# Kernel tuning notes

Measured on AMD Instinct MI355X. Metric: run time of the kernel, lower is better.

The kernel has to match this reference:

```python
import jax, jax.numpy as jnp
import numpy as np

B, C, N, T = 8, 256, 1024, 60
TW = 12  # time window size
BN_EPS = 1e-5


def _B_matrix():
    # Block-diagonal window mask: three 12x12 blocks, then one 24x24 block.
    A = np.zeros((T, T), dtype=np.float32)
    for k in range(3):
        A[k * TW:(k + 1) * TW, k * TW:(k + 1) * TW] = 1.0
    A[3 * TW:3 * TW + 2 * TW, 3 * TW:3 * TW + 2 * TW] = 1.0
    return jnp.asarray(-1e13 * (1.0 - A), dtype=jnp.float32)


def setup_inputs() -> dict:
    key = jax.random.key(0)
    ks = jax.random.split(key, 5)
    return {
        "seq": jax.random.normal(ks[0], (B, C, N, T), dtype=jnp.float32),
        "w1": jax.random.normal(ks[1], (C,), dtype=jnp.float32) * 0.05,   # conv1 weight (c_in -> 1)
        "w2": jax.random.normal(ks[2], (N,), dtype=jnp.float32) * 0.02,   # conv2 weight (num_nodes -> 1)
        "w": jax.random.normal(ks[3], (N, C), dtype=jnp.float32) * 0.03,  # xavier-ish scale
        "b": jnp.zeros((T, T), dtype=jnp.float32),
        "v": jax.random.normal(ks[4], (T, T), dtype=jnp.float32) * 0.1,
        "gamma": jnp.ones((T,), dtype=jnp.float32),
        "beta": jnp.zeros((T,), dtype=jnp.float32),
    }


def reference(seq, w1, w2, w, b, v, gamma, beta):
    # seq: [B, C, N, T]
    # conv1 over channel dim on seq.permute(0,1,3,2): f1[b,t,n] = sum_c w1[c]*seq[b,c,n,t]
    f1 = jnp.einsum('c,bcnt->btn', w1, seq)            # [B, T, N]
    # conv2 over node dim on seq.permute(0,2,1,3): f2[b,c,t] = sum_n w2[n]*seq[b,c,n,t]
    f2 = jnp.einsum('n,bcnt->bct', w2, seq)            # [B, C, T]
    logits = jax.nn.sigmoid(jnp.einsum('btn,nc,bcs->bts', f1, w, f2) + b)  # [B, T, T]
    logits = jnp.einsum('ij,bjt->bit', v, logits)      # v @ logits
    # BatchNorm1d (training mode, biased var) over channels = dim 2 after permute
    x = jnp.transpose(logits, (0, 2, 1))               # [B, T(chan), T]
    mean = x.mean(axis=(0, 2), keepdims=True)
    var = x.var(axis=(0, 2), keepdims=True)
    x = (x - mean) * jax.lax.rsqrt(var + BN_EPS) * gamma[None, :, None] + beta[None, :, None]
    logits = jnp.transpose(x, (0, 2, 1))               # [B, T, T]
    return jax.nn.softmax(logits + _B_matrix(), axis=-1)
```

## Files before the change

### kernel.cpp

```cpp
#include <hip/hip_runtime.h>
#include <cstdint>
#include <cstddef>


#define CSTRIDE 61440

typedef float vfloat4 __attribute__((ext_vector_type(4)));

__device__ __forceinline__ float quad_reduce(float x) {
    int y1 = __builtin_amdgcn_update_dpp(0, __float_as_int(x), 0xB1, 0xF, 0xF, true);
    float s1 = x + __int_as_float(y1);
    int y2 = __builtin_amdgcn_update_dpp(0, __float_as_int(s1), 0x4E, 0xF, 0xF, true);
    return s1 + __int_as_float(y2);
}

__global__ __launch_bounds__(256) void kA(const float* __restrict__ seq,
                                          const float* __restrict__ w1,
                                          const float* __restrict__ w2,
                                          float* __restrict__ f1p,
                                          float* __restrict__ f2p) {
    const int blk  = blockIdx.x;
    const int b    = blk >> 7;
    const int cg   = (blk >> 4) & 7;
    const int nc   = blk & 15;
    const int tid  = threadIdx.x;
    const int wv   = tid >> 6;
    const int lane = tid & 63;
    const int q    = lane & 3;
    const int r    = lane >> 2;
    const bool act = (r < 15);
    const int base_n = (nc << 6) + (wv << 4);
    const int c0   = cg << 5;

    __shared__ float lf2[7680];

    float w2v[4];
    #pragma unroll
    for (int j = 0; j < 4; ++j) w2v[j] = w2[base_n + 4 * j + q];

    const size_t planeOff = (size_t)(b * 256 + c0) * CSTRIDE + (size_t)((base_n + q) * 60 + 4 * r);
    const float* p0 = seq + planeOff;
    const float* p1 = p0 + (size_t)CSTRIDE;
    const float* p2 = p0 + 2 * (size_t)CSTRIDE;
    const float* p3 = p0 + 3 * (size_t)CSTRIDE;

    vfloat4 P0[4], P1[4], P2[4], P3[4];
    #pragma unroll
    for (int j = 0; j < 4; ++j) {
        P0[j] = (vfloat4)(0.f);
        P1[j] = P0[j]; P2[j] = P0[j]; P3[j] = P0[j];
    }
    if (act) {
        #pragma unroll
        for (int j = 0; j < 4; ++j) P0[j] = __builtin_nontemporal_load((const vfloat4*)(p0 + j * 240));
        #pragma unroll
        for (int j = 0; j < 4; ++j) P1[j] = __builtin_nontemporal_load((const vfloat4*)(p1 + j * 240));
        #pragma unroll
        for (int j = 0; j < 4; ++j) P2[j] = __builtin_nontemporal_load((const vfloat4*)(p2 + j * 240));
        #pragma unroll
        for (int j = 0; j < 4; ++j) P3[j] = __builtin_nontemporal_load((const vfloat4*)(p3 + j * 240));
    }
    p0 += 4 * (size_t)CSTRIDE;
    p1 += 4 * (size_t)CSTRIDE;
    p2 += 4 * (size_t)CSTRIDE;
    p3 += 4 * (size_t)CSTRIDE;

    vfloat4 acc[4];
    #pragma unroll
    for (int j = 0; j < 4; ++j) acc[j] = (vfloat4)(0.f);

#define KA_STEP(P, S, PP)                                                               \
    {                                                                                   \
        const int cc = (ii << 2) + (S);                                                 \
        const float wc = w1[c0 + cc];                                                   \
        _Pragma("unroll")                                                               \
        for (int j = 0; j < 4; ++j) acc[j] += wc * P[j];                                \
        vfloat4 f2v = w2v[0]*P[0] + w2v[1]*P[1] + w2v[2]*P[2] + w2v[3]*P[3];            \
        if (pref) {                                                                     \
            _Pragma("unroll")                                                           \
            for (int j = 0; j < 4; ++j)                                                 \
                P[j] = __builtin_nontemporal_load((const vfloat4*)((PP) + j * 240));    \
        }                                                                               \
        f2v.x = quad_reduce(f2v.x);                                                     \
        f2v.y = quad_reduce(f2v.y);                                                     \
        f2v.z = quad_reduce(f2v.z);                                                     \
        f2v.w = quad_reduce(f2v.w);                                                     \
        if (act && q == 0) {                                                            \
            *(vfloat4*)(&lf2[(cc * 4 + wv) * 60 + 4 * r]) = f2v;                        \
        }                                                                               \
    }

    for (int ii = 0; ii < 8; ++ii) {
        const bool pref = act && (ii < 7);
        KA_STEP(P0, 0, p0)
        KA_STEP(P1, 1, p1)
        KA_STEP(P2, 2, p2)
        KA_STEP(P3, 3, p3)
        p0 += 4 * (size_t)CSTRIDE;
        p1 += 4 * (size_t)CSTRIDE;
        p2 += 4 * (size_t)CSTRIDE;
        p3 += 4 * (size_t)CSTRIDE;
    }
#undef KA_STEP

    if (act) {
        float* dst = f1p + ((size_t)((cg * 8 + b) * 60 + 4 * r)) * 1024 + base_n + q;
        #pragma unroll
        for (int j = 0; j < 4; ++j) {
            dst[0 * 1024 + 4 * j] = acc[j].x;
            dst[1 * 1024 + 4 * j] = acc[j].y;
            dst[2 * 1024 + 4 * j] = acc[j].z;
            dst[3 * 1024 + 4 * j] = acc[j].w;
        }
    }

    __syncthreads();
    #pragma unroll
    for (int k = 0; k < 2; ++k) {
        const int id4 = tid + k * 256;
        if (id4 < 480) {
            const int cc = id4 / 15;
            const int p  = id4 - cc * 15;
            vfloat4 s = (vfloat4)(0.f);
            #pragma unroll
            for (int w = 0; w < 4; ++w)
                s += *(const vfloat4*)(&lf2[(cc * 4 + w) * 60 + 4 * p]);
            *(vfloat4*)(f2p + ((size_t)(b * 256 + c0 + cc) * 16 + nc) * 60 + 4 * p) = s;
        }
    }
}

__global__ __launch_bounds__(256) void K1(const float* __restrict__ f2p,
                                          const float* __restrict__ f1p,
                                          const float* __restrict__ w,
                                          float* __restrict__ f2,
                                          float* __restrict__ g1p) {
    const int blk = blockIdx.x;
    const int tid = threadIdx.x;
    if (blk < 512) {
        const int row = blk * 4 + (tid >> 6);
        const int t   = tid & 63;
        if (t >= 60) return;
        const float* src = f2p + (size_t)row * 960 + t;
        float s = 0.f;
        #pragma unroll
        for (int k = 0; k < 16; ++k) s += src[k * 60];
        f2[(size_t)row * 60 + t] = s;
    } else {
        const int blk2 = blk - 512;
        const int b    = blk2 / 60;
        const int rem  = blk2 % 60;
        const int tg   = rem >> 2;
        const int ks   = rem & 3;
        const int c    = tid;

        __shared__ float fl[1024];

        {
            const int row  = tid >> 6;
            const int col4 = tid & 63;
            const int t    = tg * 4 + row;
            vfloat4 s = (vfloat4)(0.f);
            #pragma unroll
            for (int g = 0; g < 8; ++g)
                s += *(const vfloat4*)(f1p + ((size_t)((g * 8 + b) * 60 + t)) * 1024
                                             + (ks << 8) + 4 * col4);
            *(vfloat4*)(&fl[(row << 8) + 4 * col4]) = s;
        }
        __syncthreads();

        float a0 = 0.f, a1 = 0.f, a2 = 0.f, a3 = 0.f;
        const float* wp = w + (size_t)(ks << 8) * 256 + c;
        #pragma unroll 4
        for (int n = 0; n < 256; ++n) {
            const float wv = wp[n * 256];
            a0 += fl[n] * wv;
            a1 += fl[256 + n] * wv;
            a2 += fl[512 + n] * wv;
            a3 += fl[768 + n] * wv;
        }
        float* dst = g1p + ((size_t)((ks * 8 + b) * 60 + tg * 4)) * 256 + c;
        dst[0]   = a0;
        dst[256] = a1;
        dst[512] = a2;
        dst[768] = a3;
    }
}

__global__ __launch_bounds__(256) void kD(const float* __restrict__ g1p,
                                          const float* __restrict__ f2,
                                          const float* __restrict__ bmat,
                                          float* __restrict__ logits) {
    const int bt = blockIdx.x;
    const int b  = bt / 60;
    const int t  = bt % 60;
    const int tid = threadIdx.x;
    const int cq = tid >> 6;
    const int s  = tid & 63;

    __shared__ float f2s[15364];
    __shared__ float g1r[256];
    __shared__ float red[256];

    const float* fsrc = f2 + (size_t)b * 15360;
    #pragma unroll
    for (int k = 0; k < 15; ++k) {
        const int idx = tid + k * 256;
        *(float4*)(&f2s[4 * idx]) = *(const float4*)(fsrc + 4 * idx);
    }
    if (tid < 64) {
        vfloat4 sg = (vfloat4)(0.f);
        #pragma unroll
        for (int ks = 0; ks < 4; ++ks)
            sg += *(const vfloat4*)(g1p + ((size_t)((ks * 8 + b) * 60 + t)) * 256 + 4 * tid);
        *(vfloat4*)(&g1r[4 * tid]) = sg;
    }
    __syncthreads();

    float acc = 0.f;
    #pragma unroll 8
    for (int cc = 0; cc < 64; ++cc) {
        const int c = cq * 64 + cc;
        acc += g1r[c] * f2s[c * 60 + s];
    }
    red[tid] = acc;
    __syncthreads();
    if (tid < 60) {
        const float x = red[tid] + red[64 + tid] + red[128 + tid] + red[192 + tid]
                      + bmat[t * 60 + tid];
        logits[(size_t)bt * 60 + tid] = 1.f / (1.f + __expf(-x));
    }
}

__global__ __launch_bounds__(256) void kE(const float* __restrict__ v,
                                          const float* __restrict__ logits,
                                          float* __restrict__ l2) {
    const int bi = blockIdx.x;
    const int b  = bi / 60;
    const int i  = bi % 60;
    const int tid = threadIdx.x;

    __shared__ float L[3600];
    const float* src = logits + (size_t)b * 3600;
    #pragma unroll
    for (int k = 0; k < 3; ++k) {
        const int idx = tid + k * 256;
        *(float4*)(&L[4 * idx]) = *(const float4*)(src + 4 * idx);
    }
    if (tid < 132) {
        const int idx = tid + 768;
        *(float4*)(&L[4 * idx]) = *(const float4*)(src + 4 * idx);
    }
    __syncthreads();

    if (tid < 60) {
        float acc = 0.f;
        #pragma unroll 4
        for (int j = 0; j < 60; ++j) acc += v[i * 60 + j] * L[j * 60 + tid];
        l2[(size_t)bi * 60 + tid] = acc;
    }
}

__global__ __launch_bounds__(256) void kG(const float* __restrict__ l2,
                                          const float* __restrict__ gamma,
                                          const float* __restrict__ beta,
                                          float* __restrict__ out) {
    const int bi = blockIdx.x;
    const int i  = bi % 60;
    const int tid = threadIdx.x;

    __shared__ float ps[240];
    __shared__ float pss[240];
    __shared__ float sm[60];
    __shared__ float sr[60];

    if (tid < 240) {
        const int t = tid % 60;
        const int m = tid / 60;
        float s = 0.f, ss = 0.f;
        const float* src = l2 + (size_t)(m * 120) * 60 + t;
        #pragma unroll 8
        for (int k = 0; k < 120; ++k) {
            const float x = src[k * 60];
            s  += x;
            ss += x * x;
        }
        ps[tid]  = s;
        pss[tid] = ss;
    }
    __syncthreads();
    if (tid < 60) {
        const float s   = ps[tid] + ps[60 + tid] + ps[120 + tid] + ps[180 + tid];
        const float ss  = pss[tid] + pss[60 + tid] + pss[120 + tid] + pss[180 + tid];
        const float m   = s * (1.f / 480.f);
        const float var = ss * (1.f / 480.f) - m * m;
        sm[tid] = m;
        sr[tid] = rsqrtf(var + 1e-5f);
    }
    __syncthreads();

    if (tid < 64) {
        const int t = tid;
        float x = -3.0e38f;
        if (t < 60) {
            const float val = l2[(size_t)bi * 60 + t];
            const float y   = (val - sm[t]) * sr[t] * gamma[t] + beta[t];
            const int  br   = (i < 36) ? (i / 12) : 3;
            const int  lo   = (br < 3) ? br * 12 : 36;
            const int  hi   = (br < 3) ? lo + 12 : 60;
            const bool valid = (t >= lo) && (t < hi);
            x = valid ? y : (y - 1e13f);
        }
        float mx = x;
        #pragma unroll
        for (int o = 32; o > 0; o >>= 1) mx = fmaxf(mx, __shfl_xor(mx, o));
        float e = 0.f;
        if (t < 60) e = __expf(x - mx);
        float smn = e;
        #pragma unroll
        for (int o = 32; o > 0; o >>= 1) smn += __shfl_xor(smn, o);
        if (t < 60) out[(size_t)bi * 60 + t] = e / smn;
    }
}

extern "C" void kernel_launch(void* const* d_in, const int* in_sizes, int n_in,
                              void* d_out, int out_size, void* d_ws, size_t ws_size,
                              hipStream_t stream) {
    const float* seq   = (const float*)d_in[0];
    const float* w1    = (const float*)d_in[1];
    const float* w2    = (const float*)d_in[2];
    const float* w     = (const float*)d_in[3];
    const float* bmat  = (const float*)d_in[4];
    const float* v     = (const float*)d_in[5];
    const float* gamma = (const float*)d_in[6];
    const float* beta  = (const float*)d_in[7];
    float* out = (float*)d_out;
    float* ws  = (float*)d_ws;

    float* f1p    = ws;
    float* f2p    = ws + 3932160;
    float* f2     = ws + 5898240;
    float* g1p    = ws + 6021120;
    float* logits = ws + 6512640;
    float* l2     = ws + 6541440;

    kA<<<1024, 256, 0, stream>>>(seq, w1, w2, f1p, f2p);
    K1<<<992, 256, 0, stream>>>(f2p, f1p, w, f2, g1p);
    kD<<<480, 256, 0, stream>>>(g1p, f2, bmat, logits);
    kE<<<480, 256, 0, stream>>>(v, logits, l2);
    kG<<<480, 256, 0, stream>>>(l2, gamma, beta, out);
}
```

Measured before the change: 131.8 us.

## Fuse four tail kernels into one cooperative kernel with grid syncs

Replaces the K1, kD, kE and kG launches with a single cooperative kernel that uses grid.sync() between stages, removing three kernel launch gaps. The kD stage no longer stages the per-batch f2 slab in shared memory and instead reads it directly from global memory. Shared memory is unioned into one 3600-float buffer. This relies on all 992 blocks being co-resident (launch bounds of 4 blocks per CU are declared). Grid-wide barriers add their own overhead, and the direct global reads of f2 may cost more than the old shared-memory staging.

```diff
diff --git a/kernel.cpp b/kernel.cpp
--- a/kernel.cpp
+++ b/kernel.cpp
@@ -1,6 +1,9 @@
 #include <hip/hip_runtime.h>
+#include <hip/hip_cooperative_groups.h>
 #include <cstdint>
 #include <cstddef>
+
+namespace cg = cooperative_groups;
 
 
 #define CSTRIDE 61440
@@ -21,7 +24,7 @@
                                           float* __restrict__ f2p) {
     const int blk  = blockIdx.x;
     const int b    = blk >> 7;
-    const int cg   = (blk >> 4) & 7;
+    const int cg_  = (blk >> 4) & 7;
     const int nc   = blk & 15;
     const int tid  = threadIdx.x;
     const int wv   = tid >> 6;
@@ -30,7 +33,7 @@
     const int r    = lane >> 2;
     const bool act = (r < 15);
     const int base_n = (nc << 6) + (wv << 4);
-    const int c0   = cg << 5;
+    const int c0   = cg_ << 5;
 
     __shared__ float lf2[7680];
 
@@ -104,7 +107,7 @@
 #undef KA_STEP
 
     if (act) {
-        float* dst = f1p + ((size_t)((cg * 8 + b) * 60 + 4 * r)) * 1024 + base_n + q;
+        float* dst = f1p + ((size_t)((cg_ * 8 + b) * 60 + 4 * r)) * 1024 + base_n + q;
         #pragma unroll
         for (int j = 0; j < 4; ++j) {
             dst[0 * 1024 + 4 * j] = acc[j].x;
@@ -123,29 +126,40 @@
             const int p  = id4 - cc * 15;
             vfloat4 s = (vfloat4)(0.f);
             #pragma unroll
-            for (int w = 0; w < 4; ++w)
-                s += *(const vfloat4*)(&lf2[(cc * 4 + w) * 60 + 4 * p]);
+            for (int w_ = 0; w_ < 4; ++w_)
+                s += *(const vfloat4*)(&lf2[(cc * 4 + w_) * 60 + 4 * p]);
             *(vfloat4*)(f2p + ((size_t)(b * 256 + c0 + cc) * 16 + nc) * 60 + 4 * p) = s;
         }
     }
 }
 
-__global__ __launch_bounds__(256) void K1(const float* __restrict__ f2p,
-                                          const float* __restrict__ f1p,
-                                          const float* __restrict__ w,
-                                          float* __restrict__ f2,
-                                          float* __restrict__ g1p) {
+__global__ __launch_bounds__(256, 4) void KT(const float* __restrict__ f2p,
+                                             const float* __restrict__ f1p,
+                                             const float* __restrict__ w,
+                                             const float* __restrict__ bmat,
+                                             const float* __restrict__ v,
+                                             const float* __restrict__ gamma,
+                                             const float* __restrict__ beta,
+                                             float* __restrict__ f2,
+                                             float* __restrict__ g1p,
+                                             float* __restrict__ logits,
+                                             float* __restrict__ l2,
+                                             float* __restrict__ out) {
+    cg::grid_group grid = cg::this_grid();
+    __shared__ float S[3600];
     const int blk = blockIdx.x;
     const int tid = threadIdx.x;
+
     if (blk < 512) {
         const int row = blk * 4 + (tid >> 6);
         const int t   = tid & 63;
-        if (t >= 60) return;
-        const float* src = f2p + (size_t)row * 960 + t;
-        float s = 0.f;
-        #pragma unroll
-        for (int k = 0; k < 16; ++k) s += src[k * 60];
-        f2[(size_t)row * 60 + t] = s;
+        if (t < 60) {
+            const float* src = f2p + (size_t)row * 960 + t;
+            float s = 0.f;
+            #pragma unroll
+            for (int k = 0; k < 16; ++k) s += src[k * 60];
+            f2[(size_t)row * 60 + t] = s;
+        }
     } else {
         const int blk2 = blk - 512;
         const int b    = blk2 / 60;
@@ -154,8 +168,6 @@
         const int ks   = rem & 3;
         const int c    = tid;
 
-        __shared__ float fl[1024];
-
         {
             const int row  = tid >> 6;
             const int col4 = tid & 63;
@@ -165,7 +177,7 @@
             for (int g = 0; g < 8; ++g)
                 s += *(const vfloat4*)(f1p + ((size_t)((g * 8 + b) * 60 + t)) * 1024
                                              + (ks << 8) + 4 * col4);
-            *(vfloat4*)(&fl[(row << 8) + 4 * col4]) = s;
+            *(vfloat4*)(&S[(row << 8) + 4 * col4]) = s;
         }
         __syncthreads();
 
@@ -174,10 +186,10 @@
         #pragma unroll 4
         for (int n = 0; n < 256; ++n) {
             const float wv = wp[n * 256];
-            a0 += fl[n] * wv;
-            a1 += fl[256 + n] * wv;
-            a2 += fl[512 + n] * wv;
-            a3 += fl[768 + n] * wv;
+            a0 += S[n] * wv;
+            a1 += S[256 + n] * wv;
+            a2 += S[512 + n] * wv;
+            a3 += S[768 + n] * wv;
         }
         float* dst = g1p + ((size_t)((ks * 8 + b) * 60 + tg * 4)) * 256 + c;
         dst[0]   = a0;
@@ -185,141 +197,113 @@
         dst[512] = a2;
         dst[768] = a3;
     }
-}
-
-__global__ __launch_bounds__(256) void kD(const float* __restrict__ g1p,
-                                          const float* __restrict__ f2,
-                                          const float* __restrict__ bmat,
-                                          float* __restrict__ logits) {
-    const int bt = blockIdx.x;
-    const int b  = bt / 60;
-    const int t  = bt % 60;
-    const int tid = threadIdx.x;
-    const int cq = tid >> 6;
-    const int s  = tid & 63;
-
-    __shared__ float f2s[15364];
-    __shared__ float g1r[256];
-    __shared__ float red[256];
-
-    const float* fsrc = f2 + (size_t)b * 15360;
-    #pragma unroll
-    for (int k = 0; k < 15; ++k) {
-        const int idx = tid + k * 256;
-        *(float4*)(&f2s[4 * idx]) = *(const float4*)(fsrc + 4 * idx);
-    }
-    if (tid < 64) {
-        vfloat4 sg = (vfloat4)(0.f);
-        #pragma unroll
-        for (int ks = 0; ks < 4; ++ks)
-            sg += *(const vfloat4*)(g1p + ((size_t)((ks * 8 + b) * 60 + t)) * 256 + 4 * tid);
-        *(vfloat4*)(&g1r[4 * tid]) = sg;
-    }
-    __syncthreads();
-
-    float acc = 0.f;
-    #pragma unroll 8
-    for (int cc = 0; cc < 64; ++cc) {
-        const int c = cq * 64 + cc;
-        acc += g1r[c] * f2s[c * 60 + s];
-    }
-    red[tid] = acc;
-    __syncthreads();
-    if (tid < 60) {
-        const float x = red[tid] + red[64 + tid] + red[128 + tid] + red[192 + tid]
-                      + bmat[t * 60 + tid];
-        logits[(size_t)bt * 60 + tid] = 1.f / (1.f + __expf(-x));
-    }
-}
-
-__global__ __launch_bounds__(256) void kE(const float* __restrict__ v,
-                                          const float* __restrict__ logits,
-                                          float* __restrict__ l2) {
-    const int bi = blockIdx.x;
-    const int b  = bi / 60;
-    const int i  = bi % 60;
-    const int tid = threadIdx.x;
-
-    __shared__ float L[3600];
-    const float* src = logits + (size_t)b * 3600;
-    #pragma unroll
-    for (int k = 0; k < 3; ++k) {
-        const int idx = tid + k * 256;
-        *(float4*)(&L[4 * idx]) = *(const float4*)(src + 4 * idx);
-    }
-    if (tid < 132) {
-        const int idx = tid + 768;
-        *(float4*)(&L[4 * idx]) = *(const float4*)(src + 4 * idx);
-    }
-    __syncthreads();
-
-    if (tid < 60) {
+    grid.sync();
+
+    if (blk < 480) {
+        const int b  = blk / 60;
+        const int t  = blk % 60;
+        const int cq = tid >> 6;
+        const int s  = tid & 63;
+
+        if (tid < 64) {
+            vfloat4 sg = (vfloat4)(0.f);
+            #pragma unroll
+            for (int ks = 0; ks < 4; ++ks)
+                sg += *(const vfloat4*)(g1p + ((size_t)((ks * 8 + b) * 60 + t)) * 256 + 4 * tid);
+            *(vfloat4*)(&S[4 * tid]) = sg;
+        }
+        __syncthreads();
+
         float acc = 0.f;
-        #pragma unroll 4
-        for (int j = 0; j < 60; ++j) acc += v[i * 60 + j] * L[j * 60 + tid];
-        l2[(size_t)bi * 60 + tid] = acc;
-    }
-}
-
-__global__ __launch_bounds__(256) void kG(const float* __restrict__ l2,
-                                          const float* __restrict__ gamma,
-                                          const float* __restrict__ beta,
-                                          float* __restrict__ out) {
-    const int bi = blockIdx.x;
-    const int i  = bi % 60;
-    const int tid = threadIdx.x;
-
-    __shared__ float ps[240];
-    __shared__ float pss[240];
-    __shared__ float sm[60];
-    __shared__ float sr[60];
-
-    if (tid < 240) {
-        const int t = tid % 60;
-        const int m = tid / 60;
-        float s = 0.f, ss = 0.f;
-        const float* src = l2 + (size_t)(m * 120) * 60 + t;
+        const float* fb = f2 + (size_t)b * 15360;
         #pragma unroll 8
-        for (int k = 0; k < 120; ++k) {
-            const float x = src[k * 60];
-            s  += x;
-            ss += x * x;
-        }
-        ps[tid]  = s;
-        pss[tid] = ss;
-    }
-    __syncthreads();
-    if (tid < 60) {
-        const float s   = ps[tid] + ps[60 + tid] + ps[120 + tid] + ps[180 + tid];
-        const float ss  = pss[tid] + pss[60 + tid] + pss[120 + tid] + pss[180 + tid];
-        const float m   = s * (1.f / 480.f);
-        const float var = ss * (1.f / 480.f) - m * m;
-        sm[tid] = m;
-        sr[tid] = rsqrtf(var + 1e-5f);
-    }
-    __syncthreads();
-
-    if (tid < 64) {
-        const int t = tid;
-        float x = -3.0e38f;
-        if (t < 60) {
-            const float val = l2[(size_t)bi * 60 + t];
-            const float y   = (val - sm[t]) * sr[t] * gamma[t] + beta[t];
-            const int  br   = (i < 36) ? (i / 12) : 3;
-            const int  lo   = (br < 3) ? br * 12 : 36;
-            const int  hi   = (br < 3) ? lo + 12 : 60;
-            const bool valid = (t >= lo) && (t < hi);
-            x = valid ? y : (y - 1e13f);
-        }
-        float mx = x;
-        #pragma unroll
-        for (int o = 32; o > 0; o >>= 1) mx = fmaxf(mx, __shfl_xor(mx, o));
-        float e = 0.f;
-        if (t < 60) e = __expf(x - mx);
-        float smn = e;
-        #pragma unroll
-        for (int o = 32; o > 0; o >>= 1) smn += __shfl_xor(smn, o);
-        if (t < 60) out[(size_t)bi * 60 + t] = e / smn;
+        for (int cc = 0; cc < 64; ++cc) {
+            const int c = cq * 64 + cc;
+            acc += S[c] * fb[c * 60 + s];
+        }
+        S[512 + tid] = acc;
+        __syncthreads();
+        if (tid < 60) {
+            const float x = S[512 + tid] + S[576 + tid] + S[640 + tid] + S[704 + tid]
+                          + bmat[t * 60 + tid];
+            logits[(size_t)blk * 60 + tid] = 1.f / (1.f + __expf(-x));
+        }
+    }
+    grid.sync();
+
+    if (blk < 480) {
+        const int b = blk / 60;
+        const int i = blk % 60;
+        const float* src = logits + (size_t)b * 3600;
+        #pragma unroll
+        for (int k = 0; k < 3; ++k) {
+            const int idx = tid + k * 256;
+            *(vfloat4*)(&S[4 * idx]) = *(const vfloat4*)(src + 4 * idx);
+        }
+        if (tid < 132) {
+            const int idx = tid + 768;
+            *(vfloat4*)(&S[4 * idx]) = *(const vfloat4*)(src + 4 * idx);
+        }
+        __syncthreads();
+
+        if (tid < 60) {
+            float acc = 0.f;
+            #pragma unroll 4
+            for (int j = 0; j < 60; ++j) acc += v[i * 60 + j] * S[j * 60 + tid];
+            l2[(size_t)blk * 60 + tid] = acc;
+        }
+    }
+    grid.sync();
+
+    if (blk < 480) {
+        const int i = blk % 60;
+        if (tid < 240) {
+            const int t = tid % 60;
+            const int m = tid / 60;
+            float s = 0.f, ss = 0.f;
+            const float* src = l2 + (size_t)(m * 120) * 60 + t;
+            #pragma unroll 8
+            for (int k = 0; k < 120; ++k) {
+                const float x = src[k * 60];
+                s  += x;
+                ss += x * x;
+            }
+            S[tid]       = s;
+            S[240 + tid] = ss;
+        }
+        __syncthreads();
+        if (tid < 60) {
+            const float s   = S[tid] + S[60 + tid] + S[120 + tid] + S[180 + tid];
+            const float ss  = S[240 + tid] + S[300 + tid] + S[360 + tid] + S[420 + tid];
+            const float m   = s * (1.f / 480.f);
+            const float var = ss * (1.f / 480.f) - m * m;
+            S[480 + tid] = m;
+            S[540 + tid] = rsqrtf(var + 1e-5f);
+        }
+        __syncthreads();
+
+        if (tid < 64) {
+            const int t = tid;
+            float x = -3.0e38f;
+            if (t < 60) {
+                const float val = l2[(size_t)blk * 60 + t];
+                const float y   = (val - S[480 + t]) * S[540 + t] * gamma[t] + beta[t];
+                const int  br   = (i < 36) ? (i / 12) : 3;
+                const int  lo   = (br < 3) ? br * 12 : 36;
+                const int  hi   = (br < 3) ? lo + 12 : 60;
+                const bool valid = (t >= lo) && (t < hi);
+                x = valid ? y : (y - 1e13f);
+            }
+            float mx = x;
+            #pragma unroll
+            for (int o = 32; o > 0; o >>= 1) mx = fmaxf(mx, __shfl_xor(mx, o));
+            float e = 0.f;
+            if (t < 60) e = __expf(x - mx);
+            float smn = e;
+            #pragma unroll
+            for (int o = 32; o > 0; o >>= 1) smn += __shfl_xor(smn, o);
+            if (t < 60) out[(size_t)blk * 60 + t] = e / smn;
+        }
     }
 }
 
@@ -345,8 +329,9 @@
     float* l2     = ws + 6541440;
 
     kA<<<1024, 256, 0, stream>>>(seq, w1, w2, f1p, f2p);
-    K1<<<992, 256, 0, stream>>>(f2p, f1p, w, f2, g1p);
-    kD<<<480, 256, 0, stream>>>(g1p, f2, bmat, logits);
-    kE<<<480, 256, 0, stream>>>(v, logits, l2);
-    kG<<<480, 256, 0, stream>>>(l2, gamma, beta, out);
+
+    void* args[] = { (void*)&f2p, (void*)&f1p, (void*)&w, (void*)&bmat, (void*)&v,
+                     (void*)&gamma, (void*)&beta, (void*)&f2, (void*)&g1p,
+                     (void*)&logits, (void*)&l2, (void*)&out };
+    hipLaunchCooperativeKernel((const void*)KT, dim3(992), dim3(256), args, 0, stream);
 }
```

Measured after the change: 470.1 us. +256.8%, slower.

## Fuse sigmoid-logits and v-matmul kernels into one per-batch column-chunk kernel

Applied to the files above, without the earlier changes.

Merges kD and kE into a single kernel, kDE, launched with 32 blocks. Each block handles one batch and a 15-column slice of t. The block stages f2 transposed in shared memory, computes the sigmoid logits for all 60 rows in four chunks of 16, then applies v @ S for its columns. This removes one launch and the intermediate logits round trip to global memory. In exchange, the grid drops from 480 blocks to 32, so far fewer CUs are used, and each block serially re-reads g1p from global memory.

```diff
diff --git a/kernel.cpp b/kernel.cpp
--- a/kernel.cpp
+++ b/kernel.cpp
@@ -21,7 +21,7 @@
                                           float* __restrict__ f2p) {
     const int blk  = blockIdx.x;
     const int b    = blk >> 7;
-    const int cg   = (blk >> 4) & 7;
+    const int cg_  = (blk >> 4) & 7;
     const int nc   = blk & 15;
     const int tid  = threadIdx.x;
     const int wv   = tid >> 6;
@@ -30,7 +30,7 @@
     const int r    = lane >> 2;
     const bool act = (r < 15);
     const int base_n = (nc << 6) + (wv << 4);
-    const int c0   = cg << 5;
+    const int c0   = cg_ << 5;
 
     __shared__ float lf2[7680];
 
@@ -104,7 +104,7 @@
 #undef KA_STEP
 
     if (act) {
-        float* dst = f1p + ((size_t)((cg * 8 + b) * 60 + 4 * r)) * 1024 + base_n + q;
+        float* dst = f1p + ((size_t)((cg_ * 8 + b) * 60 + 4 * r)) * 1024 + base_n + q;
         #pragma unroll
         for (int j = 0; j < 4; ++j) {
             dst[0 * 1024 + 4 * j] = acc[j].x;
@@ -123,8 +123,8 @@
             const int p  = id4 - cc * 15;
             vfloat4 s = (vfloat4)(0.f);
             #pragma unroll
-            for (int w = 0; w < 4; ++w)
-                s += *(const vfloat4*)(&lf2[(cc * 4 + w) * 60 + 4 * p]);
+            for (int w_ = 0; w_ < 4; ++w_)
+                s += *(const vfloat4*)(&lf2[(cc * 4 + w_) * 60 + 4 * p]);
             *(vfloat4*)(f2p + ((size_t)(b * 256 + c0 + cc) * 16 + nc) * 60 + 4 * p) = s;
         }
     }
@@ -187,77 +187,75 @@
     }
 }
 
-__global__ __launch_bounds__(256) void kD(const float* __restrict__ g1p,
-                                          const float* __restrict__ f2,
-                                          const float* __restrict__ bmat,
-                                          float* __restrict__ logits) {
-    const int bt = blockIdx.x;
-    const int b  = bt / 60;
-    const int t  = bt % 60;
-    const int tid = threadIdx.x;
-    const int cq = tid >> 6;
-    const int s  = tid & 63;
-
-    __shared__ float f2s[15364];
-    __shared__ float g1r[256];
-    __shared__ float red[256];
-
-    const float* fsrc = f2 + (size_t)b * 15360;
+__global__ __launch_bounds__(256) void kDE(const float* __restrict__ g1p,
+                                           const float* __restrict__ f2,
+                                           const float* __restrict__ bmat,
+                                           const float* __restrict__ v,
+                                           float* __restrict__ l2) {
+    const int blk   = blockIdx.x;
+    const int b     = blk >> 2;
+    const int tc    = blk & 3;
+    const int tbase = tc * 15;
+    const int tid   = threadIdx.x;
+
+    __shared__ float F[15][260];
+    __shared__ float Gr[16][264];
+    __shared__ float S[60][16];
+
     #pragma unroll
     for (int k = 0; k < 15; ++k) {
         const int idx = tid + k * 256;
-        *(float4*)(&f2s[4 * idx]) = *(const float4*)(fsrc + 4 * idx);
-    }
-    if (tid < 64) {
-        vfloat4 sg = (vfloat4)(0.f);
-        #pragma unroll
-        for (int ks = 0; ks < 4; ++ks)
-            sg += *(const vfloat4*)(g1p + ((size_t)((ks * 8 + b) * 60 + t)) * 256 + 4 * tid);
-        *(vfloat4*)(&g1r[4 * tid]) = sg;
+        const int c   = idx / 15;
+        const int tp  = idx % 15;
+        F[tp][c] = f2[(size_t)b * 15360 + c * 60 + tbase + tp];
     }
     __syncthreads();
 
-    float acc = 0.f;
-    #pragma unroll 8
-    for (int cc = 0; cc < 64; ++cc) {
-        const int c = cq * 64 + cc;
-        acc += g1r[c] * f2s[c * 60 + s];
-    }
-    red[tid] = acc;
-    __syncthreads();
-    if (tid < 60) {
-        const float x = red[tid] + red[64 + tid] + red[128 + tid] + red[192 + tid]
-                      + bmat[t * 60 + tid];
-        logits[(size_t)bt * 60 + tid] = 1.f / (1.f + __expf(-x));
-    }
-}
-
-__global__ __launch_bounds__(256) void kE(const float* __restrict__ v,
-                                          const float* __restrict__ logits,
-                                          float* __restrict__ l2) {
-    const int bi = blockIdx.x;
-    const int b  = bi / 60;
-    const int i  = bi % 60;
-    const int tid = threadIdx.x;
-
-    __shared__ float L[3600];
-    const float* src = logits + (size_t)b * 3600;
-    #pragma unroll
-    for (int k = 0; k < 3; ++k) {
-        const int idx = tid + k * 256;
-        *(float4*)(&L[4 * idx]) = *(const float4*)(src + 4 * idx);
-    }
-    if (tid < 132) {
-        const int idx = tid + 768;
-        *(float4*)(&L[4 * idx]) = *(const float4*)(src + 4 * idx);
-    }
-    __syncthreads();
-
-    if (tid < 60) {
-        float acc = 0.f;
-        #pragma unroll 4
-        for (int j = 0; j < 60; ++j) acc += v[i * 60 + j] * L[j * 60 + tid];
-        l2[(size_t)bi * 60 + tid] = acc;
+    const int jl = tid / 15;
+    const int tp = tid % 15;
+
+    for (int jb = 0; jb < 4; ++jb) {
+        #pragma unroll
+        for (int k = 0; k < 4; ++k) {
+            const int idx = tid + k * 256;
+            const int j   = idx >> 6;
+            const int c4  = idx & 63;
+            vfloat4 s = (vfloat4)(0.f);
+            #pragma unroll
+            for (int ks = 0; ks < 4; ++ks)
+                s += *(const vfloat4*)(g1p + ((size_t)((ks * 8 + b) * 60 + jb * 16 + j)) * 256 + 4 * c4);
+            *(vfloat4*)(&Gr[j][4 * c4]) = s;
+        }
+        __syncthreads();
+
+        if (tid < 240) {
+            float acc = 0.f;
+            #pragma unroll 8
+            for (int c4 = 0; c4 < 64; ++c4) {
+                const vfloat4 g = *(const vfloat4*)(&Gr[jl][4 * c4]);
+                const vfloat4 f = *(const vfloat4*)(&F[tp][4 * c4]);
+                acc += g.x * f.x + g.y * f.y + g.z * f.z + g.w * f.w;
+            }
+            const int j = jb * 16 + jl;
+            const float x = acc + bmat[j * 60 + tbase + tp];
+            S[j][tp] = 1.f / (1.f + __expf(-x));
+        }
+        __syncthreads();
+    }
+
+    if (tid < 240) {
+        #pragma unroll
+        for (int k = 0; k < 4; ++k) {
+            const int idx = tid + k * 240;
+            if (idx < 900) {
+                const int i  = idx / 15;
+                const int t2 = idx % 15;
+                float acc = 0.f;
+                #pragma unroll 4
+                for (int j = 0; j < 60; ++j) acc += v[i * 60 + j] * S[j][t2];
+                l2[((size_t)b * 60 + i) * 60 + tbase + t2] = acc;
+            }
+        }
     }
 }
 
@@ -337,16 +335,14 @@
     float* out = (float*)d_out;
     float* ws  = (float*)d_ws;
 
-    float* f1p    = ws;
-    float* f2p    = ws + 3932160;
-    float* f2     = ws + 5898240;
-    float* g1p    = ws + 6021120;
-    float* logits = ws + 6512640;
-    float* l2     = ws + 6541440;
+    float* f1p = ws;
+    float* f2p = ws + 3932160;
+    float* f2  = ws + 5898240;
+    float* g1p = ws + 6021120;
+    float* l2  = ws + 6541440;
 
     kA<<<1024, 256, 0, stream>>>(seq, w1, w2, f1p, f2p);
     K1<<<992, 256, 0, stream>>>(f2p, f1p, w, f2, g1p);
-    kD<<<480, 256, 0, stream>>>(g1p, f2, bmat, logits);
-    kE<<<480, 256, 0, stream>>>(v, logits, l2);
+    kDE<<<32, 256, 0, stream>>>(g1p, f2, bmat, v, l2);
     kG<<<480, 256, 0, stream>>>(l2, gamma, beta, out);
 }
```

Result: slower. 145.2 us (+10.2%).
